# Kernel optimization log

Hardware: AMD Instinct MI355X
Metric: run time of the kernel (lower is better)

The kernel has to match this reference:

```python
import jax, jax.numpy as jnp
import numpy as np

N = 4096          # number of video frames (n)
M = 1024          # input feature size (m)
D = 1024          # output_size; must equal M for the grid_sample offset math
APPERTURE = 256   # band half-width: logits with |i-j| >= APPERTURE are masked
SCALE = 0.06      # Q scaling from the original module


def _grid_sample_bilinear(img, gx, gy):
    """F.grid_sample(img[None,None], grid, mode='bilinear', align_corners=True).
    img: (H, W); gx, gy: (H, W) normalized coords in [-1, 1].
    gx indexes the W (last) axis, gy the H axis, matching torch's grid layout."""
    H, W = img.shape
    ix = (gx + 1.0) * (W - 1) * 0.5
    iy = (gy + 1.0) * (H - 1) * 0.5
    ix0 = jnp.floor(ix)
    iy0 = jnp.floor(iy)
    wx = ix - ix0  # weight for the +1 neighbor along W
    wy = iy - iy0  # weight for the +1 neighbor along H
    ix0i = jnp.clip(ix0.astype(jnp.int32), 0, W - 1)
    ix1i = jnp.clip(ix0i + 1, 0, W - 1)
    iy0i = jnp.clip(iy0.astype(jnp.int32), 0, H - 1)
    iy1i = jnp.clip(iy0i + 1, 0, H - 1)
    v00 = img[iy0i, ix0i]
    v01 = img[iy0i, ix1i]
    v10 = img[iy1i, ix0i]
    v11 = img[iy1i, ix1i]
    return (1.0 - wy) * ((1.0 - wx) * v00 + wx * v01) + wy * ((1.0 - wx) * v10 + wx * v11)


def setup_inputs() -> dict:
    key = jax.random.key(0)
    ks = jax.random.split(key, 8)
    s = 0.02
    f32 = jnp.float32
    return {
        "x": jax.random.normal(ks[0], (N, M), f32),
        "Wq": s * jax.random.normal(ks[1], (M, D), f32),
        "Wk": s * jax.random.normal(ks[2], (M, D), f32),
        "Wv": s * jax.random.normal(ks[3], (M, D), f32),
        "Wofx": s * jax.random.normal(ks[4], (D, D), f32),
        "bofx": jnp.zeros((D,), f32),
        "Wofy": s * jax.random.normal(ks[5], (D, D), f32),
        "bofy": jnp.zeros((D,), f32),
        "Wout": s * jax.random.normal(ks[6], (D, M), f32),
    }


def reference(x, Wq, Wk, Wv, Wofx, bofx, Wofy, bofy, Wout):
    H, W = x.shape  # H = n frames, W = m features
    Q = x @ Wq                       # (n, D)
    # offsets are computed from the UNscaled Q (scaling happens later in torch)
    ofx = Q @ Wofx + bofx            # (n, D) == (H, W) since D == W
    ofy = Q @ Wofy + bofy
    # base grid: channel 0 = 2*i/H - 1 (row), channel 1 = 2*j/W - 1 (col);
    # grid_sample reads channel 0 as the x (W-axis) coordinate, channel 1 as y.
    rows = jnp.arange(H, dtype=x.dtype)[:, None]
    cols = jnp.arange(W, dtype=x.dtype)[None, :]
    gx = jnp.clip(2.0 * rows / H - 1.0 + ofx, -1.0, 1.0)  # (H, W)
    gy = jnp.clip(2.0 * cols / W - 1.0 + ofy, -1.0, 1.0)  # (H, W)
    x_new = _grid_sample_bilinear(x, gx, gy)              # (H, W)
    K = x_new @ Wk                   # (n, D)
    V = x_new @ Wv                   # (n, D)
    logits = (SCALE * Q) @ K.T       # (n, n)
    idx = jnp.arange(H)
    band_mask = jnp.abs(idx[:, None] - idx[None, :]) >= APPERTURE
    logits = jnp.where(band_mask, -jnp.inf, logits)
    att = jax.nn.softmax(logits, axis=-1)  # (n, n); dropout is identity at eval
    # torch: y = (V.T @ att).T  ==  att.T @ V  (note the transpose of att!)
    y = att.T @ V                    # (n, D)
    y = y @ Wout                     # (n, m)
    return y, att
```

## Files before the change

### kernel.cpp

```cpp
#include <hip/hip_runtime.h>
#include <hip/hip_bf16.h>
#include <math.h>

#define NN 4096
#define MM 1024
#define BANDP 512

typedef float f4v __attribute__((ext_vector_type(4)));
typedef float f32x4 __attribute__((ext_vector_type(4)));
typedef short bf16x8 __attribute__((ext_vector_type(8)));
typedef short s4v __attribute__((ext_vector_type(4)));

__device__ __forceinline__ short f2b(float f) {
    union { float f; unsigned u; } v; v.f = f;
    unsigned r = v.u + 0x7fffu + ((v.u >> 16) & 1u);
    return (short)(r >> 16);
}
__device__ __forceinline__ float b2f(short s) {
    union { unsigned u; float f; } v;
    v.u = ((unsigned)(unsigned short)s) << 16;
    return v.f;
}
__device__ __forceinline__ float b2f_lo(unsigned p) {
    union { unsigned u; float f; } v; v.u = p << 16; return v.f;
}
__device__ __forceinline__ float b2f_hi(unsigned p) {
    union { unsigned u; float f; } v; v.u = p & 0xffff0000u; return v.f;
}

__device__ __forceinline__ void gl2lds16(const void* g, void* l) {
    __builtin_amdgcn_global_load_lds(
        (const __attribute__((address_space(1))) void*)g,
        (__attribute__((address_space(3))) void*)l, 16, 0, 0);
}

#define WAIT_VM8() asm volatile("s_waitcnt vmcnt(8)" ::: "memory")
#define WAIT_VM4() asm volatile("s_waitcnt vmcnt(4)" ::: "memory")
#define WAIT_VM0() asm volatile("s_waitcnt vmcnt(0)" ::: "memory")

__global__ __launch_bounds__(256)
void split_x_k(const float* __restrict__ s, short* __restrict__ h,
               short* __restrict__ l)
{
    const int i = (blockIdx.x * 256 + threadIdx.x) << 2;
    f4v v = *(const f4v*)&s[i];
    s4v hv, lv;
    #pragma unroll
    for (int q = 0; q < 4; ++q) {
        hv[q] = f2b(v[q]);
        lv[q] = f2b(v[q] - b2f(hv[q]));
    }
    *(s4v*)&h[i] = hv;
    *(s4v*)&l[i] = lv;
}

template<int Z>
__global__ __launch_bounds__(256)
void trsplit_k(const float* __restrict__ W0, const float* __restrict__ W1,
               short* __restrict__ Th, short* __restrict__ Tl)
{
    __shared__ float tile[32][33];
    const int z = (Z > 1) ? blockIdx.z : 0;
    const float* W = (z == 0) ? W0 : W1;
    short* th = Th + (size_t)z * 1024 * 1024;
    short* tl = Tl + (size_t)z * 1024 * 1024;
    const int bx = blockIdx.x << 5, by = blockIdx.y << 5;
    const int tx = threadIdx.x, ty = threadIdx.y;
    #pragma unroll
    for (int r = ty; r < 32; r += 8)
        tile[r][tx] = W[(size_t)(by + r) * MM + bx + tx];
    __syncthreads();
    #pragma unroll
    for (int r = ty; r < 32; r += 8) {
        const float v = tile[tx][r];
        const short h = f2b(v);
        th[(size_t)(bx + r) * MM + by + tx] = h;
        tl[(size_t)(bx + r) * MM + by + tx] = f2b(v - b2f(h));
    }
}

__global__ __launch_bounds__(256)
void transpose3_k(const float* __restrict__ Wk, const float* __restrict__ Wv,
                  const float* __restrict__ Wout, short* __restrict__ WkvT,
                  short* __restrict__ WoutT)
{
    __shared__ float tile[32][33];
    const int z = blockIdx.z;
    const float* W = (z == 0) ? Wk : (z == 1) ? Wv : Wout;
    short* dst = (z == 2) ? WoutT : WkvT + (size_t)z * 1024 * 1024;
    const int bx = blockIdx.x << 5, by = blockIdx.y << 5;
    const int tx = threadIdx.x, ty = threadIdx.y;
    #pragma unroll
    for (int r = ty; r < 32; r += 8)
        tile[r][tx] = W[(size_t)(by + r) * MM + bx + tx];
    __syncthreads();
    #pragma unroll
    for (int r = ty; r < 32; r += 8)
        dst[(size_t)(bx + r) * MM + by + tx] = f2b(tile[tx][r]);
}

template<bool BIAS>
__global__ __launch_bounds__(256, 2)
void gemm_split(const short* __restrict__ Ah, const short* __restrict__ Al,
                const short* __restrict__ Bth, const short* __restrict__ Btl,
                const float* __restrict__ bias0, const float* __restrict__ bias1,
                short* __restrict__ outH, short* __restrict__ outL, int N)
{
    __shared__ short As[2][2][128 * 32];
    __shared__ short Bs[2][2][128 * 32];

    const int t  = threadIdx.x;
    const int l  = t & 63;
    const int w  = t >> 6;
    const int wm = w >> 1, wn = w & 1;
    const int lr = l & 15;
    const int lk = (l >> 4) << 3;
    const int lks = lk ^ (((l >> 1) & 3) << 3);

    const int i0 = blockIdx.y << 7;
    const int bn = blockIdx.x << 7;

    const int sr = t >> 2;
    const int sk = (((t & 3) ^ ((t >> 3) & 3)) << 3);

    const short* aH = Ah  + (size_t)(i0 + sr) * MM + sk;
    const short* aL = Al  + (size_t)(i0 + sr) * MM + sk;
    const short* bH = Bth + (size_t)(bn + sr) * MM + sk;
    const short* bL = Btl + (size_t)(bn + sr) * MM + sk;

    f32x4 acc[4][4] = {};

    auto stage = [&](int sb, int k0) {
        gl2lds16(aH + k0,           &As[sb][0][t * 8]);
        gl2lds16(aH + 64 * MM + k0, &As[sb][0][2048 + t * 8]);
        gl2lds16(aL + k0,           &As[sb][1][t * 8]);
        gl2lds16(aL + 64 * MM + k0, &As[sb][1][2048 + t * 8]);
        gl2lds16(bH + k0,           &Bs[sb][0][t * 8]);
        gl2lds16(bH + 64 * MM + k0, &Bs[sb][0][2048 + t * 8]);
        gl2lds16(bL + k0,           &Bs[sb][1][t * 8]);
        gl2lds16(bL + 64 * MM + k0, &Bs[sb][1][2048 + t * 8]);
    };
    stage(0, 0);

    for (int kt = 0; kt < 32; ++kt) {
        const int cur = kt & 1;
        if (kt + 1 < 32) { stage(cur ^ 1, (kt + 1) << 5); WAIT_VM8(); }
        else             { WAIT_VM0(); }
        __builtin_amdgcn_s_barrier();
        __builtin_amdgcn_sched_barrier(0);

        bf16x8 ah[4], al[4], bh[4], bl[4];
        #pragma unroll
        for (int i = 0; i < 4; ++i) {
            ah[i] = *(const bf16x8*)&As[cur][0][(wm * 64 + i * 16 + lr) * 32 + lks];
            al[i] = *(const bf16x8*)&As[cur][1][(wm * 64 + i * 16 + lr) * 32 + lks];
        }
        #pragma unroll
        for (int j = 0; j < 4; ++j) {
            bh[j] = *(const bf16x8*)&Bs[cur][0][(wn * 64 + j * 16 + lr) * 32 + lks];
            bl[j] = *(const bf16x8*)&Bs[cur][1][(wn * 64 + j * 16 + lr) * 32 + lks];
        }
        __builtin_amdgcn_s_setprio(1);
        #pragma unroll
        for (int i = 0; i < 4; ++i)
            #pragma unroll
            for (int j = 0; j < 4; ++j) {
                acc[i][j] = __builtin_amdgcn_mfma_f32_16x16x32_bf16(ah[i], bl[j], acc[i][j], 0, 0, 0);
                acc[i][j] = __builtin_amdgcn_mfma_f32_16x16x32_bf16(al[i], bh[j], acc[i][j], 0, 0, 0);
                acc[i][j] = __builtin_amdgcn_mfma_f32_16x16x32_bf16(ah[i], bh[j], acc[i][j], 0, 0, 0);
            }
        __builtin_amdgcn_s_setprio(0);
        __builtin_amdgcn_s_barrier();
    }

    const int rb = (l >> 4) << 2;
    #pragma unroll
    for (int i = 0; i < 4; ++i)
        #pragma unroll
        for (int j = 0; j < 4; ++j) {
            const int n = bn + wn * 64 + j * 16 + lr;
            float bv = 0.f;
            if (BIAS) bv = (n < 1024) ? bias0[n] : bias1[n - 1024];
            #pragma unroll
            for (int r = 0; r < 4; ++r) {
                const int m = i0 + wm * 64 + i * 16 + rb + r;
                const float v = acc[i][j][r] + bv;
                const short h = f2b(v);
                outH[(size_t)m * N + n] = h;
                outL[(size_t)m * N + n] = f2b(v - b2f(h));
            }
        }
}

__global__ __launch_bounds__(256)
void grid_sample_k(const short* __restrict__ xh, const short* __restrict__ ofh,
                   const short* __restrict__ ofl, short* __restrict__ xnb)
{
    const int i = blockIdx.x;
    const int tid = threadIdx.x;
    const int j4 = tid << 2;

    const short* rh = ofh + (size_t)i * 2048;
    const short* rl = ofl + (size_t)i * 2048;
    s4v hx = *(const s4v*)&rh[j4];
    s4v lx = *(const s4v*)&rl[j4];
    s4v hy = *(const s4v*)&rh[1024 + j4];
    s4v ly = *(const s4v*)&rl[1024 + j4];
    s4v out;

    const float gxb = (2.0f * (float)i) / (float)NN - 1.0f;

    #pragma unroll
    for (int q = 0; q < 4; ++q) {
        const int j = j4 + q;
        float gx = gxb + b2f(hx[q]) + b2f(lx[q]);
        gx = fminf(fmaxf(gx, -1.0f), 1.0f);
        float gy = (2.0f * (float)j) / (float)MM - 1.0f + b2f(hy[q]) + b2f(ly[q]);
        gy = fminf(fmaxf(gy, -1.0f), 1.0f);

        const float ixf = (gx + 1.0f) * 511.5f;
        const float iyf = (gy + 1.0f) * 2047.5f;
        const float ix0 = floorf(ixf);
        const float iy0 = floorf(iyf);
        const float wx = ixf - ix0;
        const float wy = iyf - iy0;
        int ix0i = (int)ix0; ix0i = max(0, min(ix0i, MM - 1));
        int iy0i = (int)iy0; iy0i = max(0, min(iy0i, NN - 1));
        const int iy1i = min(iy0i + 1, NN - 1);

        const int wb = min(ix0i, MM - 2);
        const bool at_edge = ix0i > wb;

        const short* r0 = xh + (size_t)iy0i * MM + wb;
        const short* r1 = xh + (size_t)iy1i * MM + wb;
        unsigned w0, w1;
        __builtin_memcpy(&w0, r0, 4);
        __builtin_memcpy(&w1, r1, 4);

        const float v01 = b2f_hi(w0);
        const float v11 = b2f_hi(w1);
        const float v00 = at_edge ? v01 : b2f_lo(w0);
        const float v10 = at_edge ? v11 : b2f_lo(w1);

        out[q] = f2b((1.0f - wy) * ((1.0f - wx) * v00 + wx * v01)
                   + wy * ((1.0f - wx) * v10 + wx * v11));
    }
    *(s4v*)&xnb[(size_t)i * MM + j4] = out;
}

template<int MODE>
__global__ __launch_bounds__(256, 2)
void mfma_gemm(const short* __restrict__ A, const short* __restrict__ Bt,
               void* __restrict__ C0, void* __restrict__ C1)
{
    __shared__ short As[2][128 * 32];
    __shared__ short Bs[2][128 * 32];

    const int t  = threadIdx.x;
    const int l  = t & 63;
    const int w  = t >> 6;
    const int wm = w >> 1, wn = w & 1;
    const int lr = l & 15;
    const int lk = (l >> 4) << 3;
    const int lks = lk ^ (((l >> 1) & 3) << 3);

    const int i0 = blockIdx.y << 7;
    const int bn = blockIdx.x << 7;
    const int jb = (MODE == 3) ? (i0 - 256 + bn) : bn;

    const int sr = t >> 2;
    const int sk = (((t & 3) ^ ((t >> 3) & 3)) << 3);

    const short* aS = A + (size_t)(i0 + sr) * MM + sk;
    int br0 = jb + sr, br1 = jb + sr + 64;
    if (MODE == 3) {
        br0 = min(max(br0, 0), NN - 1);
        br1 = min(max(br1, 0), NN - 1);
    }
    const short* bS0 = Bt + (size_t)br0 * MM + sk;
    const short* bS1 = Bt + (size_t)br1 * MM + sk;

    f32x4 acc[4][4] = {};

    auto stage = [&](int sb, int k0) {
        gl2lds16(aS + k0,           &As[sb][0] + t * 8);
        gl2lds16(aS + 64 * MM + k0, &As[sb][0] + 2048 + t * 8);
        gl2lds16(bS0 + k0,          &Bs[sb][0] + t * 8);
        gl2lds16(bS1 + k0,          &Bs[sb][0] + 2048 + t * 8);
    };
    stage(0, 0);

    for (int kt = 0; kt < 32; ++kt) {
        const int cur = kt & 1;
        if (kt + 1 < 32) { stage(cur ^ 1, (kt + 1) << 5); WAIT_VM4(); }
        else             { WAIT_VM0(); }
        __builtin_amdgcn_s_barrier();
        __builtin_amdgcn_sched_barrier(0);

        bf16x8 a[4], b[4];
        #pragma unroll
        for (int i = 0; i < 4; ++i)
            a[i] = *(const bf16x8*)&As[cur][(wm * 64 + i * 16 + lr) * 32 + lks];
        #pragma unroll
        for (int j = 0; j < 4; ++j)
            b[j] = *(const bf16x8*)&Bs[cur][(wn * 64 + j * 16 + lr) * 32 + lks];
        __builtin_amdgcn_s_setprio(1);
        #pragma unroll
        for (int i = 0; i < 4; ++i)
            #pragma unroll
            for (int j = 0; j < 4; ++j)
                acc[i][j] = __builtin_amdgcn_mfma_f32_16x16x32_bf16(a[i], b[j], acc[i][j], 0, 0, 0);
        __builtin_amdgcn_s_setprio(0);
        __builtin_amdgcn_s_barrier();
    }

    const int rb = (l >> 4) << 2;
    #pragma unroll
    for (int i = 0; i < 4; ++i) {
        #pragma unroll
        for (int j = 0; j < 4; ++j) {
            const int nl = wn * 64 + j * 16 + lr;
            if (MODE == 4 && bn + nl >= 1024) {
                const int m0 = i0 + wm * 64 + i * 16 + rb;
                s4v o;
                #pragma unroll
                for (int r = 0; r < 4; ++r) o[r] = f2b(acc[i][j][r]);
                *(s4v*)&((short*)C1)[(size_t)(bn + nl - 1024) * NN + m0] = o;
            } else {
                #pragma unroll
                for (int r = 0; r < 4; ++r) {
                    const int m = i0 + wm * 64 + i * 16 + rb + r;
                    const float v = acc[i][j][r];
                    if (MODE == 4) {
                        ((short*)C0)[(size_t)m * MM + bn + nl] = f2b(v);
                    } else if (MODE == 2) {
                        ((float*)C0)[(size_t)m * MM + bn + nl] = v;
                    } else if (MODE == 3) {
                        const int jj = jb + nl;
                        const int ci = jj - m + 255;
                        if (ci >= 0 && ci <= 510)
                            ((float*)C0)[(size_t)m * BANDP + ci] =
                                (jj >= 0 && jj < NN) ? 0.06f * v : -INFINITY;
                    }
                }
            }
        }
    }
}

__global__ __launch_bounds__(256)
void band_softmax(const float* __restrict__ band, float* __restrict__ att,
                  short* __restrict__ bandT)
{
    const int i = blockIdx.x;
    const int tid = threadIdx.x;
    const float* brow = band + (size_t)i * BANDP;

    float v0 = brow[tid];
    float v1 = (tid < 255) ? brow[tid + 256] : -INFINITY;

    float m = fmaxf(v0, v1);
    #pragma unroll
    for (int o = 32; o >= 1; o >>= 1) m = fmaxf(m, __shfl_xor(m, o));
    __shared__ float redm[4], reds[4];
    const int wv = tid >> 6, ln = tid & 63;
    if (ln == 0) redm[wv] = m;
    __syncthreads();
    m = fmaxf(fmaxf(redm[0], redm[1]), fmaxf(redm[2], redm[3]));

    float p0 = expf(v0 - m);
    float p1 = (tid < 255) ? expf(v1 - m) : 0.f;
    float s = p0 + p1;
    #pragma unroll
    for (int o = 32; o >= 1; o >>= 1) s += __shfl_xor(s, o);
    if (ln == 0) reds[wv] = s;
    __syncthreads();
    s = reds[0] + reds[1] + reds[2] + reds[3];
    const float rinv = 1.0f / s;
    p0 *= rinv; p1 *= rinv;

    float* arow = att + (size_t)i * NN;
    f4v z = {0.f, 0.f, 0.f, 0.f};
    #pragma unroll
    for (int q = 0; q < 4; ++q)
        *(f4v*)&arow[(q * 256 + tid) << 2] = z;
    __syncthreads();
    int j = i + tid - 255;
    if (j >= 0 && j < NN) {
        arow[j] = p0;
        bandT[(size_t)j * 768 + (i - (j & ~7) + 384)] = f2b(p0);
    }
    j = i + tid + 1;
    if (tid < 255 && j >= 0 && j < NN) {
        arow[j] = p1;
        bandT[(size_t)j * 768 + (i - (j & ~7) + 384)] = f2b(p1);
    }
}

__global__ __launch_bounds__(256, 2)
void attT_v_mfma(const short* __restrict__ bandT, const short* __restrict__ Vt,
                 short* __restrict__ y1b)
{
    const int t = threadIdx.x, l = t & 63, w = t >> 6;
    const int wm = w >> 1, wn = w & 1;
    const int lr = l & 15, lk = (l >> 4) << 3;
    const int r0 = blockIdx.y << 7;
    const int n0 = blockIdx.x << 6;

    f32x4 acc[4][2] = {};
    for (int ks = 0; ks < 20; ++ks) {
        const int j0 = r0 - 256 + (ks << 5);
        if (j0 < 0 || j0 >= NN) continue;
        bf16x8 b[2];
        #pragma unroll
        for (int j = 0; j < 2; ++j)
            b[j] = *(const bf16x8*)&Vt[(size_t)(n0 + wn * 32 + j * 16 + lr) * NN + j0 + lk];
        #pragma unroll
        for (int i = 0; i < 4; ++i) {
            const int r = r0 + wm * 64 + i * 16 + lr;
            const int cc = j0 + lk - (r & ~7) + 384;
            bf16x8 a = *(const bf16x8*)&bandT[(size_t)r * 768 + cc];
            #pragma unroll
            for (int j = 0; j < 2; ++j)
                acc[i][j] = __builtin_amdgcn_mfma_f32_16x16x32_bf16(a, b[j], acc[i][j], 0, 0, 0);
        }
    }
    const int rb = (l >> 4) << 2;
    #pragma unroll
    for (int i = 0; i < 4; ++i)
        #pragma unroll
        for (int j = 0; j < 2; ++j)
            #pragma unroll
            for (int r = 0; r < 4; ++r)
                y1b[(size_t)(r0 + wm * 64 + i * 16 + rb + r) * MM + n0 + wn * 32 + j * 16 + lr]
                    = f2b(acc[i][j][r]);
}

extern "C" void kernel_launch(void* const* d_in, const int* in_sizes, int n_in,
                              void* d_out, int out_size, void* d_ws, size_t ws_size,
                              hipStream_t stream)
{
    const float* x    = (const float*)d_in[0];
    const float* Wq   = (const float*)d_in[1];
    const float* Wk   = (const float*)d_in[2];
    const float* Wv   = (const float*)d_in[3];
    const float* Wofx = (const float*)d_in[4];
    const float* bofx = (const float*)d_in[5];
    const float* Wofy = (const float*)d_in[6];
    const float* bofy = (const float*)d_in[7];
    const float* Wout = (const float*)d_in[8];

    float* y_out   = (float*)d_out;
    float* att_out = (float*)d_out + (size_t)NN * MM;

    char* wsb = (char*)d_ws;
    const size_t MB = 1024 * 1024;
    short* xh      = (short*)(wsb + 0);
    short* Qh      = (short*)(wsb + 8 * MB);
    short* Ql      = (short*)(wsb + 16 * MB);
    short* xl      = (short*)(wsb + 24 * MB);
    short* WqTh    = (short*)(wsb + 32 * MB);
    short* WqTl    = (short*)(wsb + 34 * MB);
    short* WofxyTh = (short*)(wsb + 24 * MB);
    short* WofxyTl = (short*)(wsb + 28 * MB);
    short* ofxyh   = (short*)(wsb + 32 * MB);
    short* ofxyl   = (short*)(wsb + 48 * MB);
    short* xnb     = (short*)(wsb + 16 * MB);
    short* WkvT    = (short*)(wsb + 0);
    short* WoutT   = (short*)(wsb + 4 * MB);
    short* Kb      = (short*)(wsb + 24 * MB);
    short* Vtb     = (short*)(wsb + 32 * MB);
    float* band    = (float*)(wsb + 40 * MB);
    short* bandT   = (short*)(wsb + 48 * MB);
    short* y1b     = (short*)(wsb + 16 * MB);

    const dim3 blk(256);
    const dim3 tblk(32, 8);

    split_x_k<<<dim3(4096), blk, 0, stream>>>(x, xh, xl);
    trsplit_k<1><<<dim3(32, 32, 1), tblk, 0, stream>>>(Wq, nullptr, WqTh, WqTl);
    gemm_split<false><<<dim3(8, 32), blk, 0, stream>>>(
        xh, xl, WqTh, WqTl, nullptr, nullptr, Qh, Ql, 1024);
    trsplit_k<2><<<dim3(32, 32, 2), tblk, 0, stream>>>(Wofx, Wofy, WofxyTh, WofxyTl);
    gemm_split<true><<<dim3(16, 32), blk, 0, stream>>>(
        Qh, Ql, WofxyTh, WofxyTl, bofx, bofy, ofxyh, ofxyl, 2048);

    grid_sample_k<<<dim3(NN), blk, 0, stream>>>(xh, ofxyh, ofxyl, xnb);

    transpose3_k<<<dim3(32, 32, 3), tblk, 0, stream>>>(Wk, Wv, Wout, WkvT, WoutT);

    mfma_gemm<4><<<dim3(16, 32), blk, 0, stream>>>(xnb, WkvT, Kb, Vtb);
    mfma_gemm<3><<<dim3(5, 32), blk, 0, stream>>>(Qh, Kb, band, nullptr);
    hipMemsetAsync(bandT, 0, (size_t)NN * 768 * sizeof(short), stream);
    band_softmax<<<dim3(NN), blk, 0, stream>>>(band, att_out, bandT);
    attT_v_mfma<<<dim3(16, 32), blk, 0, stream>>>(bandT, Vtb, y1b);
    mfma_gemm<2><<<dim3(8, 32), blk, 0, stream>>>(y1b, WoutT, y_out, nullptr);
}
```

Measured before the change: 311.2 us.

## Fuse input split/transpose prep kernels and zero attention matrix via memset

Merges the x bf16 split kernel and the Wq/Wofx/Wofy transpose-split kernels into a single launch, which cuts launch count and removes serialization between them. This needed a workspace layout reshuffle so the buffers no longer alias. It also drops the per-row zero fill of the 64 MB attention output inside band_softmax, along with its block barrier, and clears the whole att buffer with hipMemsetAsync instead. The memset still writes the full matrix, and the band values are then written over it in a separate pass.

```diff
diff --git a/kernel.cpp b/kernel.cpp
--- a/kernel.cpp
+++ b/kernel.cpp
@@ -39,33 +39,34 @@
 #define WAIT_VM0() asm volatile("s_waitcnt vmcnt(0)" ::: "memory")
 
 __global__ __launch_bounds__(256)
-void split_x_k(const float* __restrict__ s, short* __restrict__ h,
-               short* __restrict__ l)
-{
-    const int i = (blockIdx.x * 256 + threadIdx.x) << 2;
-    f4v v = *(const f4v*)&s[i];
-    s4v hv, lv;
-    #pragma unroll
-    for (int q = 0; q < 4; ++q) {
-        hv[q] = f2b(v[q]);
-        lv[q] = f2b(v[q] - b2f(hv[q]));
-    }
-    *(s4v*)&h[i] = hv;
-    *(s4v*)&l[i] = lv;
-}
-
-template<int Z>
-__global__ __launch_bounds__(256)
-void trsplit_k(const float* __restrict__ W0, const float* __restrict__ W1,
-               short* __restrict__ Th, short* __restrict__ Tl)
-{
+void prep_k(const float* __restrict__ x, const float* __restrict__ Wq,
+            const float* __restrict__ Wofx, const float* __restrict__ Wofy,
+            short* __restrict__ xh, short* __restrict__ xl,
+            short* __restrict__ WqTh, short* __restrict__ WqTl,
+            short* __restrict__ WofxyTh, short* __restrict__ WofxyTl)
+{
+    const int z = blockIdx.z;
+    const int tx = threadIdx.x, ty = threadIdx.y;
+    if (z >= 3) {
+        const int b = (z - 3) * 1024 + blockIdx.y * 32 + blockIdx.x;
+        const int tid = ty * 32 + tx;
+        const int i = (b * 256 + tid) << 2;
+        f4v v = *(const f4v*)&x[i];
+        s4v hv, lv;
+        #pragma unroll
+        for (int q = 0; q < 4; ++q) {
+            hv[q] = f2b(v[q]);
+            lv[q] = f2b(v[q] - b2f(hv[q]));
+        }
+        *(s4v*)&xh[i] = hv;
+        *(s4v*)&xl[i] = lv;
+        return;
+    }
     __shared__ float tile[32][33];
-    const int z = (Z > 1) ? blockIdx.z : 0;
-    const float* W = (z == 0) ? W0 : W1;
-    short* th = Th + (size_t)z * 1024 * 1024;
-    short* tl = Tl + (size_t)z * 1024 * 1024;
+    const float* W = (z == 0) ? Wq : (z == 1) ? Wofx : Wofy;
+    short* th = (z == 0) ? WqTh : WofxyTh + (size_t)(z - 1) * 1024 * 1024;
+    short* tl = (z == 0) ? WqTl : WofxyTl + (size_t)(z - 1) * 1024 * 1024;
     const int bx = blockIdx.x << 5, by = blockIdx.y << 5;
-    const int tx = threadIdx.x, ty = threadIdx.y;
     #pragma unroll
     for (int r = ty; r < 32; r += 8)
         tile[r][tx] = W[(size_t)(by + r) * MM + bx + tx];
@@ -380,11 +381,6 @@
     p0 *= rinv; p1 *= rinv;
 
     float* arow = att + (size_t)i * NN;
-    f4v z = {0.f, 0.f, 0.f, 0.f};
-    #pragma unroll
-    for (int q = 0; q < 4; ++q)
-        *(f4v*)&arow[(q * 256 + tid) << 2] = z;
-    __syncthreads();
     int j = i + tid - 255;
     if (j >= 0 && j < NN) {
         arow[j] = p0;
@@ -458,30 +454,30 @@
     short* xh      = (short*)(wsb + 0);
     short* Qh      = (short*)(wsb + 8 * MB);
     short* Ql      = (short*)(wsb + 16 * MB);
-    short* xl      = (short*)(wsb + 24 * MB);
-    short* WqTh    = (short*)(wsb + 32 * MB);
-    short* WqTl    = (short*)(wsb + 34 * MB);
     short* WofxyTh = (short*)(wsb + 24 * MB);
     short* WofxyTl = (short*)(wsb + 28 * MB);
+    short* xl      = (short*)(wsb + 32 * MB);
+    short* WqTh    = (short*)(wsb + 40 * MB);
+    short* WqTl    = (short*)(wsb + 42 * MB);
     short* ofxyh   = (short*)(wsb + 32 * MB);
     short* ofxyl   = (short*)(wsb + 48 * MB);
     short* xnb     = (short*)(wsb + 16 * MB);
-    short* WkvT    = (short*)(wsb + 0);
-    short* WoutT   = (short*)(wsb + 4 * MB);
-    short* Kb      = (short*)(wsb + 24 * MB);
-    short* Vtb     = (short*)(wsb + 32 * MB);
-    float* band    = (float*)(wsb + 40 * MB);
-    short* bandT   = (short*)(wsb + 48 * MB);
+    short* WkvT    = (short*)(wsb + 24 * MB);
+    short* WoutT   = (short*)(wsb + 28 * MB);
+    short* Kb      = (short*)(wsb + 32 * MB);
+    short* Vtb     = (short*)(wsb + 40 * MB);
+    float* band    = (float*)(wsb + 48 * MB);
+    short* bandT   = (short*)(wsb + 56 * MB);
     short* y1b     = (short*)(wsb + 16 * MB);
 
     const dim3 blk(256);
     const dim3 tblk(32, 8);
 
-    split_x_k<<<dim3(4096), blk, 0, stream>>>(x, xh, xl);
-    trsplit_k<1><<<dim3(32, 32, 1), tblk, 0, stream>>>(Wq, nullptr, WqTh, WqTl);
+    prep_k<<<dim3(32, 32, 7), tblk, 0, stream>>>(
+        x, Wq, Wofx, Wofy, xh, xl, WqTh, WqTl, WofxyTh, WofxyTl);
+
     gemm_split<false><<<dim3(8, 32), blk, 0, stream>>>(
         xh, xl, WqTh, WqTl, nullptr, nullptr, Qh, Ql, 1024);
-    trsplit_k<2><<<dim3(32, 32, 2), tblk, 0, stream>>>(Wofx, Wofy, WofxyTh, WofxyTl);
     gemm_split<true><<<dim3(16, 32), blk, 0, stream>>>(
         Qh, Ql, WofxyTh, WofxyTl, bofx, bofy, ofxyh, ofxyl, 2048);
 
@@ -491,6 +487,7 @@
 
     mfma_gemm<4><<<dim3(16, 32), blk, 0, stream>>>(xnb, WkvT, Kb, Vtb);
     mfma_gemm<3><<<dim3(5, 32), blk, 0, stream>>>(Qh, Kb, band, nullptr);
+    hipMemsetAsync(att_out, 0, (size_t)NN * NN * sizeof(float), stream);
     hipMemsetAsync(bandT, 0, (size_t)NN * 768 * sizeof(short), stream);
     band_softmax<<<dim3(NN), blk, 0, stream>>>(band, att_out, bandT);
     attT_v_mfma<<<dim3(16, 32), blk, 0, stream>>>(bandT, Vtb, y1b);
```

After: 310.0 us. About the same (-0.4%).
